# Performance work log

Measured on AMD Instinct MI355X. Metric: run time of the kernel, lower is better.

The kernel has to match this reference:

```python
import jax, jax.numpy as jnp
import numpy as np

INPUT_DIM = 128
OUTPUT_DIM = 256
BATCH = 4096

def setup_inputs() -> dict:
    key = jax.random.key(0)
    k_x, k_w1, k_b1, k_w2, k_b2 = jax.random.split(key, 5)
    d = INPUT_DIM
    h = 2 * OUTPUT_DIM
    x = jax.random.normal(k_x, (BATCH, d), dtype=jnp.float32)
    # Linear weights stored as [in, out]; scale ~ torch default init
    W1 = jax.random.uniform(k_w1, (d * d, h), dtype=jnp.float32, minval=-1, maxval=1) / np.sqrt(d * d)
    b1 = jax.random.uniform(k_b1, (h,), dtype=jnp.float32, minval=-1, maxval=1) / np.sqrt(d * d)
    W2 = jax.random.uniform(k_w2, (h, OUTPUT_DIM), dtype=jnp.float32, minval=-1, maxval=1) / np.sqrt(h)
    b2 = jax.random.uniform(k_b2, (OUTPUT_DIM,), dtype=jnp.float32, minval=-1, maxval=1) / np.sqrt(h)
    return {"x": x, "W1": W1, "b1": b1, "W2": W2, "b2": b2}

def reference(x, W1, b1, W2, b2):
    B, d = x.shape
    # torch bmm of the two expanded copies: tp[b,i,j] = sum_k x[b,i]*x[b,j] = d * x[b,i]*x[b,j]
    tp = jnp.asarray(d, x.dtype) * jnp.einsum('bi,bj->bij', x, x)  # [B, d, d]
    flat = tp.reshape(B, d * d)
    h = jax.nn.relu(flat @ W1 + b1)  # [B, 2*output_dim]
    return h @ W2 + b2               # [B, output_dim]
```

## Files before the change

### kernel.cpp

```cpp
#include <hip/hip_runtime.h>
#include <hip/hip_bf16.h>


typedef __attribute__((ext_vector_type(8))) short short8;
typedef __attribute__((ext_vector_type(4))) float floatx4;

__device__ __forceinline__ unsigned short f2bf(float f) {
    union { float f; unsigned int u; } v; v.f = f;
    unsigned int r = v.u + 0x7fffu + ((v.u >> 16) & 1u);
    return (unsigned short)(r >> 16);
}
__device__ __forceinline__ float bf2f(unsigned short b) {
    union { unsigned int u; float f; } v; v.u = ((unsigned int)b) << 16;
    return v.f;
}

__global__ __launch_bounds__(256) void pack_w1_kernel(
    const float* __restrict__ W1, unsigned short* __restrict__ W1Tp) {
    __shared__ float tile[64][65];
    const int k0 = blockIdx.x * 64;
    const int c0 = blockIdx.y * 64;
    const int tr = threadIdx.x >> 4;
    const int tc4 = (threadIdx.x & 15) * 4;
#pragma unroll
    for (int p = 0; p < 4; ++p) {
        int k = p * 16 + tr;
        float4 v = *(const float4*)(W1 + (long)(k0 + k) * 512 + c0 + tc4);
        tile[k][tc4 + 0] = v.x; tile[k][tc4 + 1] = v.y;
        tile[k][tc4 + 2] = v.z; tile[k][tc4 + 3] = v.w;
    }
    __syncthreads();
    const int lane = threadIdx.x & 63;
    const int w = threadIdx.x >> 6;
    const int m = lane & 15, quad = lane >> 4;
#pragma unroll
    for (int pass = 0; pass < 2; ++pass) {
        int chunk = w * 2 + pass;
        int kcL = chunk & 1, c16L = chunk >> 1;
        union { unsigned short s[8]; uint4 u; } o;
#pragma unroll
        for (int j = 0; j < 8; ++j)
            o.s[j] = f2bf(tile[kcL * 32 + quad * 8 + j][c16L * 16 + m]);
        long c16g = (c0 >> 4) + c16L;
        long kcg  = (k0 >> 5) + kcL;
        *(uint4*)(W1Tp + (c16g * 512 + kcg) * 512 + lane * 8) = o.u;
    }
}

__global__ __launch_bounds__(256) void transpose_cast_kernel(
    const float* __restrict__ in, unsigned short* __restrict__ out, int R, int C) {
    __shared__ float tile[64][65];
    const int r0 = blockIdx.x * 64, c0 = blockIdx.y * 64;
    const int tr = threadIdx.x >> 4;
    const int tc4 = (threadIdx.x & 15) * 4;
#pragma unroll
    for (int p = 0; p < 4; ++p) {
        int r = p * 16 + tr;
        float4 v = *(const float4*)(in + (long)(r0 + r) * C + c0 + tc4);
        tile[r][tc4 + 0] = v.x; tile[r][tc4 + 1] = v.y;
        tile[r][tc4 + 2] = v.z; tile[r][tc4 + 3] = v.w;
    }
    __syncthreads();
#pragma unroll
    for (int p = 0; p < 4; ++p) {
        int c = p * 16 + tr;
        union { unsigned short s[4]; uint2 u; } pk;
#pragma unroll
        for (int e = 0; e < 4; ++e) pk.s[e] = f2bf(tile[tc4 + e][c]);
        *(uint2*)(out + (long)(c0 + c) * R + r0 + tc4) = pk.u;
    }
}

__global__ __launch_bounds__(256, 4) void gemm1_kernel(
    const float* __restrict__ x,
    const unsigned short* __restrict__ W1Tp,
    float* __restrict__ partials) {
    __shared__ unsigned short xT[32][136];
    const int tid = threadIdx.x;
    const int b0 = blockIdx.x * 128;
    const int c0 = blockIdx.y * 64;
    const int i0 = blockIdx.z * 32;

    for (int idx = tid; idx < 32 * 128; idx += 256) {
        int iL = idx & 31, bL = idx >> 5;
        xT[iL][bL] = f2bf(x[(long)(b0 + bL) * 128 + i0 + iL]);
    }
    __syncthreads();

    const int wid = tid >> 6;
    const int wm = wid >> 1, wn = wid & 1;
    const int lane = tid & 63;
    const int n16 = lane & 15, quad = lane >> 4;
    const int bBase = b0 + wn * 64;
    const int c16base = (c0 >> 4) + wm * 2;

    floatx4 acc[2][4];
#pragma unroll
    for (int tm = 0; tm < 2; ++tm)
#pragma unroll
        for (int tn = 0; tn < 4; ++tn) acc[tm][tn] = (floatx4){0.f, 0.f, 0.f, 0.f};
    const floatx4 zero4 = (floatx4){0.f, 0.f, 0.f, 0.f};

#pragma unroll
    for (int jh = 0; jh < 2; ++jh) {
        short8 Xf[2][4];
#pragma unroll
        for (int ks = 0; ks < 2; ++ks)
#pragma unroll
            for (int tn = 0; tn < 4; ++tn) {
                const float* xp = x + (long)(bBase + tn * 16 + n16) * 128
                                    + jh * 64 + ks * 32 + quad * 8;
                float4 v0 = *(const float4*)xp;
                float4 v1 = *(const float4*)(xp + 4);
                short8 f;
                f[0] = (short)f2bf(v0.x); f[1] = (short)f2bf(v0.y);
                f[2] = (short)f2bf(v0.z); f[3] = (short)f2bf(v0.w);
                f[4] = (short)f2bf(v1.x); f[5] = (short)f2bf(v1.y);
                f[6] = (short)f2bf(v1.z); f[7] = (short)f2bf(v1.w);
                Xf[ks][tn] = f;
            }
        const unsigned short* aBase[2][2];
#pragma unroll
        for (int tm = 0; tm < 2; ++tm)
#pragma unroll
            for (int ks = 0; ks < 2; ++ks)
                aBase[tm][ks] = W1Tp
                    + ((long)(c16base + tm) * 512 + (long)i0 * 4 + jh * 2 + ks) * 512
                    + lane * 8;

        short8 Abuf[2][2][2];
#pragma unroll
        for (int tm = 0; tm < 2; ++tm)
#pragma unroll
            for (int ks = 0; ks < 2; ++ks) {
                Abuf[0][tm][ks] = *(const short8*)(aBase[tm][ks]);
                Abuf[1][tm][ks] = *(const short8*)(aBase[tm][ks] + 2048);
            }
#pragma unroll 4
        for (int i = 0; i < 32; ++i) {
            const int st = i & 1;
            float xi[4];
#pragma unroll
            for (int tn = 0; tn < 4; ++tn)
                xi[tn] = bf2f(xT[i][wn * 64 + tn * 16 + n16]);
#pragma unroll
            for (int tm = 0; tm < 2; ++tm)
#pragma unroll
                for (int tn = 0; tn < 4; ++tn) {
                    floatx4 t = __builtin_amdgcn_mfma_f32_16x16x32_bf16(
                        Abuf[st][tm][0], Xf[0][tn], zero4, 0, 0, 0);
                    t = __builtin_amdgcn_mfma_f32_16x16x32_bf16(
                        Abuf[st][tm][1], Xf[1][tn], t, 0, 0, 0);
                    acc[tm][tn] += xi[tn] * t;
                }
            const int pi = (i + 2) & 31;
#pragma unroll
            for (int tm = 0; tm < 2; ++tm)
#pragma unroll
                for (int ks = 0; ks < 2; ++ks)
                    Abuf[st][tm][ks] =
                        *(const short8*)(aBase[tm][ks] + (long)pi * 2048);
        }
    }

    float* pbase = partials + (long)blockIdx.z * (512L * 4096);
#pragma unroll
    for (int tm = 0; tm < 2; ++tm)
#pragma unroll
        for (int tn = 0; tn < 4; ++tn)
#pragma unroll
            for (int r = 0; r < 4; ++r) {
                int c = (c16base + tm) * 16 + quad * 4 + r;
                int b = bBase + tn * 16 + n16;
                pbase[(long)c * 4096 + b] = acc[tm][tn][r];
            }
}

__global__ __launch_bounds__(256) void tail_kernel(
    const float* __restrict__ partials,
    const float* __restrict__ b1,
    const unsigned short* __restrict__ W2T,
    const float* __restrict__ b2,
    float* __restrict__ out) {
    __shared__ unsigned short hL[32][516];
    __shared__ float b1s[512];
    const int tid = threadIdx.x;
    const int b0 = blockIdx.x * 32;
    b1s[tid] = b1[tid];
    b1s[tid + 256] = b1[tid + 256];
    __syncthreads();

    const int bL = tid & 31;
    const int cr = tid >> 5;
    const long P = 512L * 4096;
#pragma unroll 4
    for (int cp = cr; cp < 256; cp += 8) {
        int c = cp * 2;
        long off0 = (long)c * 4096 + b0 + bL;
        float s0 = partials[off0] + partials[off0 + P]
                 + partials[off0 + 2 * P] + partials[off0 + 3 * P];
        long off1 = off0 + 4096;
        float s1 = partials[off1] + partials[off1 + P]
                 + partials[off1 + 2 * P] + partials[off1 + 3 * P];
        float v0 = fmaxf(fmaf(128.f, s0, b1s[c]), 0.f);
        float v1 = fmaxf(fmaf(128.f, s1, b1s[c + 1]), 0.f);
        unsigned int pk = (unsigned int)f2bf(v0) | ((unsigned int)f2bf(v1) << 16);
        *(unsigned int*)&hL[bL][c] = pk;
    }
    __syncthreads();

    const int w = tid >> 6, lane = tid & 63;
    const int n16 = lane & 15, quad = lane >> 4;
    const int o0 = w * 64;
    floatx4 acc[2][4];
#pragma unroll
    for (int tm = 0; tm < 2; ++tm)
#pragma unroll
        for (int tn = 0; tn < 4; ++tn) acc[tm][tn] = (floatx4){0.f, 0.f, 0.f, 0.f};

#pragma unroll 4
    for (int ks = 0; ks < 16; ++ks) {
        short8 Af[2], Bf[4];
#pragma unroll
        for (int tm = 0; tm < 2; ++tm) {
            const unsigned short* p = &hL[tm * 16 + n16][ks * 32 + quad * 8];
            union { uint2 u[2]; short8 s; } cvt;
            cvt.u[0] = *(const uint2*)p;
            cvt.u[1] = *(const uint2*)(p + 4);
            Af[tm] = cvt.s;
        }
#pragma unroll
        for (int tn = 0; tn < 4; ++tn)
            Bf[tn] = *(const short8*)(W2T + (long)(o0 + tn * 16 + n16) * 512
                                      + ks * 32 + quad * 8);
#pragma unroll
        for (int tm = 0; tm < 2; ++tm)
#pragma unroll
            for (int tn = 0; tn < 4; ++tn)
                acc[tm][tn] = __builtin_amdgcn_mfma_f32_16x16x32_bf16(
                    Af[tm], Bf[tn], acc[tm][tn], 0, 0, 0);
    }
#pragma unroll
    for (int tn = 0; tn < 4; ++tn) {
        float bias = b2[o0 + tn * 16 + n16];
#pragma unroll
        for (int tm = 0; tm < 2; ++tm)
#pragma unroll
            for (int r = 0; r < 4; ++r)
                out[(long)(b0 + tm * 16 + quad * 4 + r) * 256
                    + o0 + tn * 16 + n16] = acc[tm][tn][r] + bias;
    }
}

extern "C" void kernel_launch(void* const* d_in, const int* in_sizes, int n_in,
                              void* d_out, int out_size, void* d_ws, size_t ws_size,
                              hipStream_t stream) {
    const float* x  = (const float*)d_in[0];
    const float* W1 = (const float*)d_in[1];
    const float* b1 = (const float*)d_in[2];
    const float* W2 = (const float*)d_in[3];
    const float* b2 = (const float*)d_in[4];
    float* out = (float*)d_out;

    char* ws = (char*)d_ws;
    unsigned short* W1Tp = (unsigned short*)(ws);
    unsigned short* W2T  = (unsigned short*)(ws + 16777216);
    float*          parts = (float*)(ws + 16777216 + 262144);

    pack_w1_kernel<<<dim3(256, 8), 256, 0, stream>>>(W1, W1Tp);
    transpose_cast_kernel<<<dim3(8, 4), 256, 0, stream>>>(W2, W2T, 512, 256);
    gemm1_kernel<<<dim3(32, 8, 4), 256, 0, stream>>>(x, W1Tp, parts);
    tail_kernel<<<dim3(128), 256, 0, stream>>>(parts, b1, W2T, b2, out);
}
```

Measured before the change: 177.9 us.

## Remap gemm1 grid to 1D, batch xT LDS reads, halve tail tile

Measured after the change: 215.3 us. 21.0% more time.

```diff
diff --git a/kernel.cpp b/kernel.cpp
--- a/kernel.cpp
+++ b/kernel.cpp
@@ -75,15 +75,16 @@
     const float* __restrict__ x,
     const unsigned short* __restrict__ W1Tp,
     float* __restrict__ partials) {
-    __shared__ unsigned short xT[32][136];
+    __shared__ unsigned short xT[128][40];
     const int tid = threadIdx.x;
-    const int b0 = blockIdx.x * 128;
-    const int c0 = blockIdx.y * 64;
-    const int i0 = blockIdx.z * 32;
-
-    for (int idx = tid; idx < 32 * 128; idx += 256) {
-        int iL = idx & 31, bL = idx >> 5;
-        xT[iL][bL] = f2bf(x[(long)(b0 + bL) * 128 + i0 + iL]);
+    const int n = blockIdx.x;
+    const int c0 = (n & 7) * 64;
+    const int i0 = ((n >> 3) & 3) * 32;
+    const int b0 = (n >> 5) * 128;
+
+    for (int idx = tid; idx < 128 * 32; idx += 256) {
+        int bL = idx >> 5, iL = idx & 31;
+        xT[bL][iL] = f2bf(x[(long)(b0 + bL) * 128 + i0 + iL]);
     }
     __syncthreads();
 
@@ -93,6 +94,7 @@
     const int n16 = lane & 15, quad = lane >> 4;
     const int bBase = b0 + wn * 64;
     const int c16base = (c0 >> 4) + wm * 2;
+    const int bLloc = wn * 64 + n16;
 
     floatx4 acc[2][4];
 #pragma unroll
@@ -136,13 +138,22 @@
                 Abuf[0][tm][ks] = *(const short8*)(aBase[tm][ks]);
                 Abuf[1][tm][ks] = *(const short8*)(aBase[tm][ks] + 2048);
             }
+
+        uint2 xiB[4];
 #pragma unroll 4
         for (int i = 0; i < 32; ++i) {
             const int st = i & 1;
+            if ((i & 3) == 0) {
+#pragma unroll
+                for (int tn = 0; tn < 4; ++tn)
+                    xiB[tn] = *(const uint2*)&xT[bLloc + tn * 16][i];
+            }
             float xi[4];
 #pragma unroll
-            for (int tn = 0; tn < 4; ++tn)
-                xi[tn] = bf2f(xT[i][wn * 64 + tn * 16 + n16]);
+            for (int tn = 0; tn < 4; ++tn) {
+                const unsigned short* sp = (const unsigned short*)&xiB[tn];
+                xi[tn] = bf2f(sp[i & 3]);
+            }
 #pragma unroll
             for (int tm = 0; tm < 2; ++tm)
 #pragma unroll
@@ -163,7 +174,7 @@
         }
     }
 
-    float* pbase = partials + (long)blockIdx.z * (512L * 4096);
+    float* pbase = partials + (long)((n >> 3) & 3) * (512L * 4096);
 #pragma unroll
     for (int tm = 0; tm < 2; ++tm)
 #pragma unroll
@@ -182,19 +193,19 @@
     const unsigned short* __restrict__ W2T,
     const float* __restrict__ b2,
     float* __restrict__ out) {
-    __shared__ unsigned short hL[32][516];
+    __shared__ unsigned short hL[16][516];
     __shared__ float b1s[512];
     const int tid = threadIdx.x;
-    const int b0 = blockIdx.x * 32;
+    const int b0 = blockIdx.x * 16;
     b1s[tid] = b1[tid];
     b1s[tid + 256] = b1[tid + 256];
     __syncthreads();
 
-    const int bL = tid & 31;
-    const int cr = tid >> 5;
+    const int bL = tid & 15;
+    const int cr = tid >> 4;
     const long P = 512L * 4096;
 #pragma unroll 4
-    for (int cp = cr; cp < 256; cp += 8) {
+    for (int cp = cr; cp < 256; cp += 16) {
         int c = cp * 2;
         long off0 = (long)c * 4096 + b0 + bL;
         float s0 = partials[off0] + partials[off0 + P]
@@ -212,43 +223,36 @@
     const int w = tid >> 6, lane = tid & 63;
     const int n16 = lane & 15, quad = lane >> 4;
     const int o0 = w * 64;
-    floatx4 acc[2][4];
-#pragma unroll
-    for (int tm = 0; tm < 2; ++tm)
-#pragma unroll
-        for (int tn = 0; tn < 4; ++tn) acc[tm][tn] = (floatx4){0.f, 0.f, 0.f, 0.f};
+    floatx4 acc[4];
+#pragma unroll
+    for (int tn = 0; tn < 4; ++tn) acc[tn] = (floatx4){0.f, 0.f, 0.f, 0.f};
 
 #pragma unroll 4
     for (int ks = 0; ks < 16; ++ks) {
-        short8 Af[2], Bf[4];
-#pragma unroll
-        for (int tm = 0; tm < 2; ++tm) {
-            const unsigned short* p = &hL[tm * 16 + n16][ks * 32 + quad * 8];
+        short8 Af, Bf[4];
+        {
+            const unsigned short* p = &hL[n16][ks * 32 + quad * 8];
             union { uint2 u[2]; short8 s; } cvt;
             cvt.u[0] = *(const uint2*)p;
             cvt.u[1] = *(const uint2*)(p + 4);
-            Af[tm] = cvt.s;
+            Af = cvt.s;
         }
 #pragma unroll
         for (int tn = 0; tn < 4; ++tn)
             Bf[tn] = *(const short8*)(W2T + (long)(o0 + tn * 16 + n16) * 512
                                       + ks * 32 + quad * 8);
 #pragma unroll
-        for (int tm = 0; tm < 2; ++tm)
-#pragma unroll
-            for (int tn = 0; tn < 4; ++tn)
-                acc[tm][tn] = __builtin_amdgcn_mfma_f32_16x16x32_bf16(
-                    Af[tm], Bf[tn], acc[tm][tn], 0, 0, 0);
+        for (int tn = 0; tn < 4; ++tn)
+            acc[tn] = __builtin_amdgcn_mfma_f32_16x16x32_bf16(
+                Af, Bf[tn], acc[tn], 0, 0, 0);
     }
 #pragma unroll
     for (int tn = 0; tn < 4; ++tn) {
         float bias = b2[o0 + tn * 16 + n16];
 #pragma unroll
-        for (int tm = 0; tm < 2; ++tm)
-#pragma unroll
-            for (int r = 0; r < 4; ++r)
-                out[(long)(b0 + tm * 16 + quad * 4 + r) * 256
-                    + o0 + tn * 16 + n16] = acc[tm][tn][r] + bias;
+        for (int r = 0; r < 4; ++r)
+            out[(long)(b0 + quad * 4 + r) * 256
+                + o0 + tn * 16 + n16] = acc[tn][r] + bias;
     }
 }
 
@@ -269,6 +273,6 @@
 
     pack_w1_kernel<<<dim3(256, 8), 256, 0, stream>>>(W1, W1Tp);
     transpose_cast_kernel<<<dim3(8, 4), 256, 0, stream>>>(W2, W2T, 512, 256);
-    gemm1_kernel<<<dim3(32, 8, 4), 256, 0, stream>>>(x, W1Tp, parts);
-    tail_kernel<<<dim3(128), 256, 0, stream>>>(parts, b1, W2T, b2, out);
-}
+    gemm1_kernel<<<dim3(1024), 256, 0, stream>>>(x, W1Tp, parts);
+    tail_kernel<<<dim3(256), 256, 0, stream>>>(parts, b1, W2T, b2, out);
+}
```
